# Kernel optimization log

Hardware: AMD Instinct MI355X
Metric: run time of the kernel (lower is better)

The kernel has to match this reference:

```python
import jax, jax.numpy as jnp
import numpy as np

HIDDEN = 4096
NUM_EXPERTS = 64
TOP_K = 2
N_TOKENS = 16384


def setup_inputs() -> dict:
    key = jax.random.key(0)
    kx, kw = jax.random.split(key)
    x = jax.random.normal(kx, (N_TOKENS, HIDDEN), dtype=jnp.float32)
    # nn.Linear(hidden, num_experts, bias=False) weight: [num_experts, hidden]
    gate_w = jax.random.normal(kw, (NUM_EXPERTS, HIDDEN), dtype=jnp.float32) * (HIDDEN ** -0.5)
    return {"x": x, "gate_w": gate_w}


def reference(x, gate_w):
    # logits: [N, num_experts]
    logits = jnp.einsum("nh,eh->ne", x, gate_w)
    topk_vals, topk_idx = jax.lax.top_k(logits, TOP_K)  # [N, k]
    topk_gates = jax.nn.softmax(topk_vals, axis=-1)
    return topk_gates, topk_idx
```

## Files before the change

kernel.cpp:

```cpp
#include <hip/hip_runtime.h>

#define NTOK 16384
#define HID  4096
#define NEXP 64
#define BM   32
#define BK   64
#define NSTEPS (HID / BK)

typedef _Float16 f16;
typedef f16  f16x8 __attribute__((ext_vector_type(8)));
typedef float f32x4 __attribute__((ext_vector_type(4)));

__device__ __forceinline__ int swz(int row, int u) {
    return row * 64 + ((u ^ (row & 7)) << 3);
}

__global__ __launch_bounds__(256)
void topk_gate_kernel(const float* __restrict__ x,
                      const float* __restrict__ w,
                      float* __restrict__ out) {
    __shared__ __align__(16) f16 Ah[BM * BK];
    __shared__ __align__(16) f16 Al[BM * BK];
    __shared__ __align__(16) f16 Bh[NEXP * BK];
    __shared__ __align__(16) f16 Bl[NEXP * BK];
    __shared__ float red[2][BM][4];

    const int t    = threadIdx.x;
    const int blk  = blockIdx.x;
    const int lane = t & 63;
    const int wid  = t >> 6;
    const int wm   = wid & 1;
    const int wn   = wid >> 1;
    const int col  = lane & 15;
    const int grp  = lane >> 4;

    const int  arow_s = t >> 3;
    const int  ao     = t & 7;
    const float* asrc = x + ((size_t)blk * BM + arow_s) * HID + ao * 8;
    const int  brow_s = t >> 2;
    const int  bq     = t & 3;
    const float* bsrc = w + (size_t)brow_s * HID + bq * 16;

    f32x4 acc0 = {0.f, 0.f, 0.f, 0.f};
    f32x4 acc1 = {0.f, 0.f, 0.f, 0.f};

    float4 ca[2], cb[4];
    #pragma unroll
    for (int i = 0; i < 2; ++i) ca[i] = *(const float4*)(asrc + i * 4);
    #pragma unroll
    for (int i = 0; i < 4; ++i) cb[i] = *(const float4*)(bsrc + i * 4);

    for (int s = 0; s < NSTEPS; ++s) {
        const int sn = (s + 1 < NSTEPS) ? (s + 1) : s;
        float4 na[2], nb[4];
        #pragma unroll
        for (int i = 0; i < 2; ++i) na[i] = *(const float4*)(asrc + (size_t)sn * BK + i * 4);
        #pragma unroll
        for (int i = 0; i < 4; ++i) nb[i] = *(const float4*)(bsrc + (size_t)sn * BK + i * 4);

        __syncthreads();

        {
            float v[8] = {ca[0].x, ca[0].y, ca[0].z, ca[0].w,
                          ca[1].x, ca[1].y, ca[1].z, ca[1].w};
            f16x8 hi, lo;
            #pragma unroll
            for (int j = 0; j < 8; ++j) {
                f16 h = (f16)v[j];
                hi[j] = h;
                lo[j] = (f16)(v[j] - (float)h);
            }
            int off = swz(arow_s, ao);
            *(f16x8*)&Ah[off] = hi;
            *(f16x8*)&Al[off] = lo;
        }
        #pragma unroll
        for (int j2 = 0; j2 < 2; ++j2) {
            float4 a = cb[2 * j2], b = cb[2 * j2 + 1];
            float v[8] = {a.x, a.y, a.z, a.w, b.x, b.y, b.z, b.w};
            f16x8 hi, lo;
            #pragma unroll
            for (int j = 0; j < 8; ++j) {
                float sv = v[j] * 64.0f;
                f16 h = (f16)sv;
                hi[j] = h;
                lo[j] = (f16)(sv - (float)h);
            }
            int off = swz(brow_s, 2 * bq + j2);
            *(f16x8*)&Bh[off] = hi;
            *(f16x8*)&Bl[off] = lo;
        }
        __syncthreads();

        const int arow  = wm * 16 + col;
        const int brow0 = wn * 32 + col;
        const int brow1 = brow0 + 16;
        #pragma unroll
        for (int ks = 0; ks < 2; ++ks) {
            int u = ks * 4 + grp;
            f16x8 ah  = *(const f16x8*)&Ah[swz(arow,  u)];
            f16x8 al  = *(const f16x8*)&Al[swz(arow,  u)];
            f16x8 b0h = *(const f16x8*)&Bh[swz(brow0, u)];
            f16x8 b0l = *(const f16x8*)&Bl[swz(brow0, u)];
            f16x8 b1h = *(const f16x8*)&Bh[swz(brow1, u)];
            f16x8 b1l = *(const f16x8*)&Bl[swz(brow1, u)];
            acc0 = __builtin_amdgcn_mfma_f32_16x16x32_f16(ah, b0h, acc0, 0, 0, 0);
            acc0 = __builtin_amdgcn_mfma_f32_16x16x32_f16(ah, b0l, acc0, 0, 0, 0);
            acc0 = __builtin_amdgcn_mfma_f32_16x16x32_f16(al, b0h, acc0, 0, 0, 0);
            acc1 = __builtin_amdgcn_mfma_f32_16x16x32_f16(ah, b1h, acc1, 0, 0, 0);
            acc1 = __builtin_amdgcn_mfma_f32_16x16x32_f16(ah, b1l, acc1, 0, 0, 0);
            acc1 = __builtin_amdgcn_mfma_f32_16x16x32_f16(al, b1h, acc1, 0, 0, 0);
        }

        #pragma unroll
        for (int i = 0; i < 2; ++i) ca[i] = na[i];
        #pragma unroll
        for (int i = 0; i < 4; ++i) cb[i] = nb[i];
    }

    #pragma unroll
    for (int r = 0; r < 4; ++r) {
        float va = acc0[r], vb = acc1[r];
        int   ia = wn * 32 + col, ib = ia + 16;
        float v0, v1; int i0, i1;
        if (va >= vb) { v0 = va; i0 = ia; v1 = vb; i1 = ib; }
        else          { v0 = vb; i0 = ib; v1 = va; i1 = ia; }
        #pragma unroll
        for (int m = 1; m <= 8; m <<= 1) {
            float ov0 = __shfl_xor(v0, m, 64);
            int   oi0 = __shfl_xor(i0, m, 64);
            float ov1 = __shfl_xor(v1, m, 64);
            int   oi1 = __shfl_xor(i1, m, 64);
            bool ob = (ov0 > v0) || (ov0 == v0 && oi0 < i0);
            if (ob) {
                bool k2 = (v0 > ov1) || (v0 == ov1 && i0 < oi1);
                v1 = k2 ? v0 : ov1; i1 = k2 ? i0 : oi1;
                v0 = ov0; i0 = oi0;
            } else {
                bool k2 = (ov0 > v1) || (ov0 == v1 && oi0 < i1);
                v1 = k2 ? ov0 : v1; i1 = k2 ? oi0 : i1;
            }
        }
        if (col == 0) {
            int tl = wm * 16 + grp * 4 + r;
            red[wn][tl][0] = v0; red[wn][tl][1] = (float)i0;
            red[wn][tl][2] = v1; red[wn][tl][3] = (float)i1;
        }
    }
    __syncthreads();

    if (t < BM) {
        float v0 = red[0][t][0]; int i0 = (int)red[0][t][1];
        float v1 = red[0][t][2]; int i1 = (int)red[0][t][3];
        float b0 = red[1][t][0]; int bi0 = (int)red[1][t][1];
        float b1 = red[1][t][2]; int bi1 = (int)red[1][t][3];
        bool bb = (b0 > v0) || (b0 == v0 && bi0 < i0);
        if (bb) {
            bool k2 = (v0 > b1) || (v0 == b1 && i0 < bi1);
            float nv1 = k2 ? v0 : b1; int ni1 = k2 ? i0 : bi1;
            v0 = b0; i0 = bi0; v1 = nv1; i1 = ni1;
        } else {
            bool k2 = (b0 > v1) || (b0 == v1 && bi0 < i1);
            v1 = k2 ? b0 : v1; i1 = k2 ? bi0 : i1;
        }
        float d  = (v1 - v0) * (1.0f / 64.0f);
        float e  = expf(d);
        float g0 = 1.0f / (1.0f + e);
        float g1 = e / (1.0f + e);

        int tok = blk * BM + t;
        out[(size_t)tok * 2 + 0] = g0;
        out[(size_t)tok * 2 + 1] = g1;
        out[(size_t)NTOK * 2 + (size_t)tok * 2 + 0] = (float)i0;
        out[(size_t)NTOK * 2 + (size_t)tok * 2 + 1] = (float)i1;
    }
}

extern "C" void kernel_launch(void* const* d_in, const int* in_sizes, int n_in,
                              void* d_out, int out_size, void* d_ws, size_t ws_size,
                              hipStream_t stream) {
    const float* x = (const float*)d_in[0];
    const float* w = (const float*)d_in[1];
    float* out = (float*)d_out;
    (void)in_sizes; (void)n_in; (void)out_size; (void)d_ws; (void)ws_size;

    topk_gate_kernel<<<dim3(NTOK / BM), dim3(256), 0, stream>>>(x, w, out);
}
```

Measured before the change: 74.22 us.

## Prepack gate weights to fp16 hi/lo and stream them via async LDS loads

A small pre-kernel converts the fp32 gate weights once per call into scaled fp16 hi/lo halves, laid out in the swizzled LDS order and stored in the workspace. The main kernel no longer has every block redo this conversion. It fetches each weight tile with global_load_lds DMA into a triple-buffered LDS ring, issued two steps ahead so the copies overlap the MFMA work. This removes redundant VALU conversion and register staging of B, at the cost of an extra launch, 48KB of LDS for B, and reliance on the asynchronous loads finishing before the next barrier.

```diff
diff --git a/kernel.cpp b/kernel.cpp
--- a/kernel.cpp
+++ b/kernel.cpp
@@ -1,28 +1,56 @@
 #include <hip/hip_runtime.h>
+#include <stdint.h>
 
 #define NTOK 16384
 #define HID  4096
 #define NEXP 64
 #define BM   32
 #define BK   64
-#define NSTEPS (HID / BK)
+#define NSTEPS 64
 
 typedef _Float16 f16;
 typedef f16  f16x8 __attribute__((ext_vector_type(8)));
 typedef float f32x4 __attribute__((ext_vector_type(4)));
 
+typedef __attribute__((address_space(3))) uint32_t  lds_u32;
+typedef __attribute__((address_space(1))) const uint32_t glb_u32;
+
 __device__ __forceinline__ int swz(int row, int u) {
     return row * 64 + ((u ^ (row & 7)) << 3);
 }
 
 __global__ __launch_bounds__(256)
+void pack_w_kernel(const float* __restrict__ w, f16* __restrict__ wp) {
+    int tid = blockIdx.x * 256 + threadIdx.x;
+    int e  = tid >> 9;
+    int k8 = tid & 511;
+    int k  = k8 << 3;
+    const float* src = w + (size_t)e * HID + k;
+    float4 v0 = *(const float4*)(src);
+    float4 v1 = *(const float4*)(src + 4);
+    float sv[8] = {v0.x, v0.y, v0.z, v0.w, v1.x, v1.y, v1.z, v1.w};
+    f16x8 hi, lo;
+    #pragma unroll
+    for (int j = 0; j < 8; ++j) {
+        float s = sv[j] * 64.0f;
+        f16 h = (f16)s;
+        hi[j] = h;
+        lo[j] = (f16)(s - (float)h);
+    }
+    int s = k >> 6;
+    int u = (k >> 3) & 7;
+    int c = 8 * e + (u ^ (e & 7));
+    *(f16x8*)&wp[(size_t)(s * 1024 + c) * 8]       = hi;
+    *(f16x8*)&wp[(size_t)(s * 1024 + 512 + c) * 8] = lo;
+}
+
+__global__ __launch_bounds__(256)
 void topk_gate_kernel(const float* __restrict__ x,
-                      const float* __restrict__ w,
+                      const f16* __restrict__ wp,
                       float* __restrict__ out) {
     __shared__ __align__(16) f16 Ah[BM * BK];
     __shared__ __align__(16) f16 Al[BM * BK];
-    __shared__ __align__(16) f16 Bh[NEXP * BK];
-    __shared__ __align__(16) f16 Bl[NEXP * BK];
+    __shared__ __align__(16) f16 Bbuf[3][2][NEXP * BK];
     __shared__ float red[2][BM][4];
 
     const int t    = threadIdx.x;
@@ -34,35 +62,40 @@
     const int col  = lane & 15;
     const int grp  = lane >> 4;
 
-    const int  arow_s = t >> 3;
-    const int  ao     = t & 7;
+    const int arow_s = t >> 3;
+    const int ao     = t & 7;
     const float* asrc = x + ((size_t)blk * BM + arow_s) * HID + ao * 8;
-    const int  brow_s = t >> 2;
-    const int  bq     = t & 3;
-    const float* bsrc = w + (size_t)brow_s * HID + bq * 16;
+    const int aoff_w = swz(arow_s, ao);
+
+    #define STAGE(s_, slot_) do {                                               \
+        _Pragma("unroll")                                                       \
+        for (int i_ = 0; i_ < 4; ++i_) {                                        \
+            int cb_ = wid * 4 + i_;                                             \
+            __builtin_amdgcn_global_load_lds(                                   \
+                (glb_u32*)(const void*)(wp +                                    \
+                    ((size_t)(s_) * 1024 + cb_ * 64 + lane) * 8),               \
+                (lds_u32*)(void*)((char*)&Bbuf[slot_][0][0] + cb_ * 1024),      \
+                16, 0, 0);                                                      \
+        }                                                                       \
+    } while (0)
 
     f32x4 acc0 = {0.f, 0.f, 0.f, 0.f};
     f32x4 acc1 = {0.f, 0.f, 0.f, 0.f};
 
-    float4 ca[2], cb[4];
-    #pragma unroll
-    for (int i = 0; i < 2; ++i) ca[i] = *(const float4*)(asrc + i * 4);
-    #pragma unroll
-    for (int i = 0; i < 4; ++i) cb[i] = *(const float4*)(bsrc + i * 4);
+    STAGE(0, 0);
+    STAGE(1, 1);
+    float4 ca0 = *(const float4*)(asrc);
+    float4 ca1 = *(const float4*)(asrc + 4);
+
+    const int arow  = wm * 16 + col;
+    const int brow0 = wn * 32 + col;
+    const int brow1 = brow0 + 16;
 
     for (int s = 0; s < NSTEPS; ++s) {
-        const int sn = (s + 1 < NSTEPS) ? (s + 1) : s;
-        float4 na[2], nb[4];
-        #pragma unroll
-        for (int i = 0; i < 2; ++i) na[i] = *(const float4*)(asrc + (size_t)sn * BK + i * 4);
-        #pragma unroll
-        for (int i = 0; i < 4; ++i) nb[i] = *(const float4*)(bsrc + (size_t)sn * BK + i * 4);
-
         __syncthreads();
 
         {
-            float v[8] = {ca[0].x, ca[0].y, ca[0].z, ca[0].w,
-                          ca[1].x, ca[1].y, ca[1].z, ca[1].w};
+            float v[8] = {ca0.x, ca0.y, ca0.z, ca0.w, ca1.x, ca1.y, ca1.z, ca1.w};
             f16x8 hi, lo;
             #pragma unroll
             for (int j = 0; j < 8; ++j) {
@@ -70,40 +103,28 @@
                 hi[j] = h;
                 lo[j] = (f16)(v[j] - (float)h);
             }
-            int off = swz(arow_s, ao);
-            *(f16x8*)&Ah[off] = hi;
-            *(f16x8*)&Al[off] = lo;
-        }
-        #pragma unroll
-        for (int j2 = 0; j2 < 2; ++j2) {
-            float4 a = cb[2 * j2], b = cb[2 * j2 + 1];
-            float v[8] = {a.x, a.y, a.z, a.w, b.x, b.y, b.z, b.w};
-            f16x8 hi, lo;
-            #pragma unroll
-            for (int j = 0; j < 8; ++j) {
-                float sv = v[j] * 64.0f;
-                f16 h = (f16)sv;
-                hi[j] = h;
-                lo[j] = (f16)(sv - (float)h);
-            }
-            int off = swz(brow_s, 2 * bq + j2);
-            *(f16x8*)&Bh[off] = hi;
-            *(f16x8*)&Bl[off] = lo;
+            *(f16x8*)&Ah[aoff_w] = hi;
+            *(f16x8*)&Al[aoff_w] = lo;
         }
         __syncthreads();
 
-        const int arow  = wm * 16 + col;
-        const int brow0 = wn * 32 + col;
-        const int brow1 = brow0 + 16;
+        if (s + 2 < NSTEPS) STAGE(s + 2, (s + 2) % 3);
+        const int sn = (s + 1 < NSTEPS) ? (s + 1) : s;
+        float4 na0 = *(const float4*)(asrc + (size_t)sn * BK);
+        float4 na1 = *(const float4*)(asrc + (size_t)sn * BK + 4);
+
+        const int slot = s % 3;
+        const f16* BhS = &Bbuf[slot][0][0];
+        const f16* BlS = &Bbuf[slot][1][0];
         #pragma unroll
         for (int ks = 0; ks < 2; ++ks) {
             int u = ks * 4 + grp;
             f16x8 ah  = *(const f16x8*)&Ah[swz(arow,  u)];
             f16x8 al  = *(const f16x8*)&Al[swz(arow,  u)];
-            f16x8 b0h = *(const f16x8*)&Bh[swz(brow0, u)];
-            f16x8 b0l = *(const f16x8*)&Bl[swz(brow0, u)];
-            f16x8 b1h = *(const f16x8*)&Bh[swz(brow1, u)];
-            f16x8 b1l = *(const f16x8*)&Bl[swz(brow1, u)];
+            f16x8 b0h = *(const f16x8*)&BhS[swz(brow0, u)];
+            f16x8 b0l = *(const f16x8*)&BlS[swz(brow0, u)];
+            f16x8 b1h = *(const f16x8*)&BhS[swz(brow1, u)];
+            f16x8 b1l = *(const f16x8*)&BlS[swz(brow1, u)];
             acc0 = __builtin_amdgcn_mfma_f32_16x16x32_f16(ah, b0h, acc0, 0, 0, 0);
             acc0 = __builtin_amdgcn_mfma_f32_16x16x32_f16(ah, b0l, acc0, 0, 0, 0);
             acc0 = __builtin_amdgcn_mfma_f32_16x16x32_f16(al, b0h, acc0, 0, 0, 0);
@@ -112,10 +133,7 @@
             acc1 = __builtin_amdgcn_mfma_f32_16x16x32_f16(al, b1h, acc1, 0, 0, 0);
         }
 
-        #pragma unroll
-        for (int i = 0; i < 2; ++i) ca[i] = na[i];
-        #pragma unroll
-        for (int i = 0; i < 4; ++i) cb[i] = nb[i];
+        ca0 = na0; ca1 = na1;
     }
 
     #pragma unroll
@@ -182,7 +200,9 @@
     const float* x = (const float*)d_in[0];
     const float* w = (const float*)d_in[1];
     float* out = (float*)d_out;
-    (void)in_sizes; (void)n_in; (void)out_size; (void)d_ws; (void)ws_size;
-
-    topk_gate_kernel<<<dim3(NTOK / BM), dim3(256), 0, stream>>>(x, w, out);
-}
+    f16* wp = (f16*)d_ws;
+    (void)in_sizes; (void)n_in; (void)out_size; (void)ws_size;
+
+    pack_w_kernel<<<dim3(128), dim3(256), 0, stream>>>(w, wp);
+    topk_gate_kernel<<<dim3(NTOK / BM), dim3(256), 0, stream>>>(x, wp, out);
+}
```

Result: slower. 97.57 us (+31.4%).
